# Optimization experiments

Hardware: AMD Instinct MI355X
Metric: run time of the kernel (lower is better)

Reference implementation:

```python
import jax, jax.numpy as jnp
import numpy as np

NEG_INF = -9e15  # matches torch's -9000000000000000.0 mask value
ALPHA = 0.2      # LeakyReLU negative slope


def setup_inputs() -> dict:
    key = jax.random.key(0)
    k1, k2, k3, k4 = jax.random.split(key, 4)
    B, N, Fin, Fout, H = 32, 512, 256, 64, 8
    x = jax.random.normal(k1, (B, N, Fin), dtype=jnp.float32)
    adj = (jax.random.uniform(k2, (B, N, N)) < 0.5).astype(jnp.float32)
    # W: Linear(in_features, out_features*n_heads, bias=False) weight, stored as (Fin, Fout*H)
    W = jax.random.normal(k3, (Fin, Fout * H), dtype=jnp.float32) / np.sqrt(Fin).astype(np.float32)
    # a: attention vector per head over concat(src,dst) features -> (H, 2*Fout)
    a = jax.random.normal(k4, (H, 2 * Fout), dtype=jnp.float32) * 0.1
    return {"x": x, "adj": adj, "W": W, "a": a}


def reference(x, adj, W, a):
    # x: (B,N,Fin), adj: (B,N,N), W: (Fin, H*F), a: (H, 2F)
    B, N, _ = x.shape
    H, twoF = a.shape
    F = twoF // 2
    h = (x @ W).reshape(B, N, H, F)  # (B,N,H,F)
    # Decompose concat-score: e_ij = lrelu(h_i . a_src + h_j . a_dst) -- same math
    # as (cat(h_i,h_j) * a).sum(-1) without materializing (B,N,N,H,2F).
    s_src = jnp.einsum('bnhf,hf->bnh', h, a[:, :F])  # (B,N,H)
    s_dst = jnp.einsum('bnhf,hf->bnh', h, a[:, F:])  # (B,N,H)
    e = s_src[:, :, None, :] + s_dst[:, None, :, :]  # (B,N,N,H)
    e = jax.nn.leaky_relu(e, negative_slope=ALPHA)
    e = jnp.where(adj[..., None] > 0, e, NEG_INF)
    attn = jax.nn.softmax(e, axis=2)  # softmax over neighbors j (dim=2)
    # dropout omitted (eval mode / p effectively 0 for the reference baseline)
    h_prime = jnp.einsum('bijh,bjhf->bihf', attn, h)  # (B,N,H,F)
    return h_prime.reshape(B, N, H * F)  # concat=True
```

## Files before the change

kernel.cpp:

```cpp
#include <hip/hip_runtime.h>
#include <hip/hip_bf16.h>
#include <stdint.h>


#define ALPHA  0.2f
#define ESCALE 1.4426950408889634f

typedef __bf16 bf16x8 __attribute__((ext_vector_type(8)));
typedef __bf16 bf16x4 __attribute__((ext_vector_type(4)));
typedef float  f32x4  __attribute__((ext_vector_type(4)));

#if __has_builtin(__builtin_amdgcn_exp2f)
#define EXP2(x) __builtin_amdgcn_exp2f(x)
#else
#define EXP2(x) exp2f(x)
#endif

#define HT_STRIDE 520
#define WT_STRIDE 264

__device__ inline bf16x8 ld8(const float* p) {
    float4 a0 = *(const float4*)p;
    float4 a1 = *(const float4*)(p + 4);
    bf16x8 r;
    r[0]=(__bf16)a0.x; r[1]=(__bf16)a0.y; r[2]=(__bf16)a0.z; r[3]=(__bf16)a0.w;
    r[4]=(__bf16)a1.x; r[5]=(__bf16)a1.y; r[6]=(__bf16)a1.z; r[7]=(__bf16)a1.w;
    return r;
}

__global__ __launch_bounds__(512) void k0_mask(const float* __restrict__ adj,
                                               unsigned* __restrict__ mask) {
    const int T2 = blockIdx.x * 512 + threadIdx.x;
    const int w    = T2 & 3;
    const int quad = (T2 >> 2) & 3;
    const int row  = (T2 >> 4) & 511;
    const int b    = T2 >> 13;
    const float* p = adj + ((long)b * 512 + row) * 512 + quad * 8;
    unsigned word = 0;
    #pragma unroll
    for (int k = 0; k < 4; ++k) {
        const float* qp = p + (w * 4 + k) * 32;
        float4 a0 = *(const float4*)qp;
        float4 a1 = *(const float4*)(qp + 4);
        unsigned byte =  (a0.x > 0.f ? 1u : 0u)
                      | ((a0.y > 0.f ? 1u : 0u) << 1)
                      | ((a0.z > 0.f ? 1u : 0u) << 2)
                      | ((a0.w > 0.f ? 1u : 0u) << 3)
                      | ((a1.x > 0.f ? 1u : 0u) << 4)
                      | ((a1.y > 0.f ? 1u : 0u) << 5)
                      | ((a1.z > 0.f ? 1u : 0u) << 6)
                      | ((a1.w > 0.f ? 1u : 0u) << 7);
        word |= byte << (8 * k);
    }
    mask[T2] = word;
}

struct SmemK1 {
    __bf16 WT[64][WT_STRIDE];
    float  asrc[64], adst[64];
};

__global__ __launch_bounds__(512, 4) void k1_gemm(const float* __restrict__ x,
                                                  const float* __restrict__ W,
                                                  const float* __restrict__ a,
                                                  __bf16* __restrict__ hT,
                                                  float* __restrict__ ssrc,
                                                  float* __restrict__ sdst) {
    __shared__ SmemK1 sm;
    const int b = blockIdx.x, h = blockIdx.y;
    const int tid  = threadIdx.x;
    const int wave = tid >> 6, lane = tid & 63;
    const int quad = lane >> 4, col = lane & 15;

    if (tid < 128) {
        float v = a[h * 128 + tid] * ESCALE;
        if (tid < 64) sm.asrc[tid] = v; else sm.adst[tid - 64] = v;
    }
    {
        int c = tid & 63, k0 = tid >> 6;
        #pragma unroll 4
        for (int t = 0; t < 32; ++t)
            sm.WT[c][k0 + t * 8] = (__bf16)W[(long)(k0 + t * 8) * 512 + h * 64 + c];
    }
    __syncthreads();

    f32x4 acc[4][4] = {};
    {
        const float* xb = x + (long)b * 512 * 256;
        for (int ks = 0; ks < 8; ++ks) {
            int k0 = ks * 32 + quad * 8;
            bf16x8 av[4], bv[4];
            #pragma unroll
            for (int it = 0; it < 4; ++it)
                av[it] = ld8(xb + (long)(wave * 64 + it * 16 + col) * 256 + k0);
            #pragma unroll
            for (int nt = 0; nt < 4; ++nt)
                bv[nt] = *(const bf16x8*)(&sm.WT[nt * 16 + col][k0]);
            #pragma unroll
            for (int it = 0; it < 4; ++it)
                #pragma unroll
                for (int nt = 0; nt < 4; ++nt)
                    acc[it][nt] = __builtin_amdgcn_mfma_f32_16x16x32_bf16(av[it], bv[nt], acc[it][nt], 0, 0, 0);
        }
    }

    const long bh = (long)b * 8 + h;
    {
        #pragma unroll
        for (int it = 0; it < 4; ++it)
            #pragma unroll
            for (int nt = 0; nt < 4; ++nt) {
                int f = nt * 16 + col;
                int j = wave * 64 + it * 16 + quad * 4;
                bf16x4 pk = { (__bf16)acc[it][nt][0], (__bf16)acc[it][nt][1],
                              (__bf16)acc[it][nt][2], (__bf16)acc[it][nt][3] };
                *(bf16x4*)(hT + (bh * 64 + f) * HT_STRIDE + j) = pk;
            }
    }

    {
        float asr[4], adr[4];
        #pragma unroll
        for (int nt = 0; nt < 4; ++nt) {
            asr[nt] = sm.asrc[nt * 16 + col];
            adr[nt] = sm.adst[nt * 16 + col];
        }
        #pragma unroll
        for (int it = 0; it < 4; ++it)
            #pragma unroll
            for (int r = 0; r < 4; ++r) {
                float ps = 0.f, pd = 0.f;
                #pragma unroll
                for (int nt = 0; nt < 4; ++nt) {
                    ps += acc[it][nt][r] * asr[nt];
                    pd += acc[it][nt][r] * adr[nt];
                }
                #pragma unroll
                for (int m = 1; m <= 8; m <<= 1) {
                    ps += __shfl_xor(ps, m, 64);
                    pd += __shfl_xor(pd, m, 64);
                }
                if (col == 0) {
                    int j = wave * 64 + it * 16 + quad * 4 + r;
                    ssrc[bh * 512 + j] = ps;
                    sdst[bh * 512 + j] = pd;
                }
            }
    }
}

struct SmemK2 {
    __bf16 hT[64][HT_STRIDE];
    float  sds[512];
};

__global__ __launch_bounds__(512, 4) void k2_attn(const uint4* __restrict__ mask,
                                                  const __bf16* __restrict__ hT,
                                                  const float* __restrict__ ssrc,
                                                  const float* __restrict__ sdst,
                                                  float* __restrict__ out) {
    __shared__ SmemK2 sm;
    const int b = blockIdx.x, h = blockIdx.y, q = blockIdx.z;
    const int tid  = threadIdx.x;
    const int wave = tid >> 6, lane = tid & 63;
    const int quad = lane >> 4, col = lane & 15;
    const long bh = (long)b * 8 + h;
    const int rowbase = q * 256 + wave * 32;

    {
        const uint4* src = (const uint4*)(hT + bh * 64 * HT_STRIDE);
        uint4* dst = (uint4*)&sm.hT[0][0];
        #pragma unroll
        for (int t = 0; t < 8; ++t)
            dst[t * 512 + tid] = src[t * 512 + tid];
        if (tid < 64) dst[4096 + tid] = src[4096 + tid];
    }
    sm.sds[tid] = sdst[bh * 512 + tid];

    float si[2]; uint4 mk[2];
    #pragma unroll
    for (int it = 0; it < 2; ++it) {
        int i = rowbase + it * 16 + col;
        si[it] = ssrc[bh * 512 + i];
        mk[it] = mask[((long)b * 512 + i) * 4 + quad];
    }
    __syncthreads();

    bf16x8 ones;
    #pragma unroll
    for (int u = 0; u < 8; ++u) ones[u] = (__bf16)1.0f;

    f32x4 acc[2][4] = {};
    f32x4 accs[2]   = {};

    #pragma unroll
    for (int ks = 0; ks < 16; ++ks) {
        const int j0 = ks * 32 + quad * 8;
        f32x4 s0 = *(const f32x4*)&sm.sds[j0];
        f32x4 s1 = *(const f32x4*)&sm.sds[j0 + 4];
        float sd[8] = {s0[0],s0[1],s0[2],s0[3],s1[0],s1[1],s1[2],s1[3]};
        unsigned mb[2];
        #pragma unroll
        for (int it = 0; it < 2; ++it) {
            unsigned wrd = (ks < 4) ? mk[it].x : (ks < 8) ? mk[it].y
                         : (ks < 12) ? mk[it].z : mk[it].w;
            mb[it] = (wrd >> ((ks & 3) * 8)) & 0xFFu;
        }
        bf16x8 P[2];
        #pragma unroll
        for (int it = 0; it < 2; ++it)
            #pragma unroll
            for (int u = 0; u < 8; ++u) {
                float e = si[it] + sd[u];
                float l = fmaxf(e, ALPHA * e);
                float xv = EXP2(l);
                P[it][u] = (__bf16)(((mb[it] >> u) & 1u) ? xv : 0.0f);
            }
        bf16x8 bv[4];
        #pragma unroll
        for (int nt = 0; nt < 4; ++nt)
            bv[nt] = *(const bf16x8*)(&sm.hT[nt * 16 + col][j0]);
        #pragma unroll
        for (int it = 0; it < 2; ++it) {
            #pragma unroll
            for (int nt = 0; nt < 4; ++nt)
                acc[it][nt] = __builtin_amdgcn_mfma_f32_16x16x32_bf16(P[it], bv[nt], acc[it][nt], 0, 0, 0);
            accs[it] = __builtin_amdgcn_mfma_f32_16x16x32_bf16(P[it], ones, accs[it], 0, 0, 0);
        }
    }
    #pragma unroll
    for (int it = 0; it < 2; ++it)
        #pragma unroll
        for (int r = 0; r < 4; ++r) {
            float s = accs[it][r];
            float inv = (s > 0.f) ? 1.0f / s : 0.f;
            int i = rowbase + it * 16 + quad * 4 + r;
            float* orow = out + ((long)b * 512 + i) * 512 + h * 64;
            #pragma unroll
            for (int nt = 0; nt < 4; ++nt)
                orow[nt * 16 + col] = acc[it][nt][r] * inv;
        }
}

struct SmemF {
    __bf16 hT[64][HT_STRIDE];
    __bf16 WT[64][WT_STRIDE];
    float  ssrc[512], sdst[512];
    float  asrc[64], adst[64];
};

__global__ __launch_bounds__(1024, 4) void k_gat_fused(const float* __restrict__ x,
                                                       const float* __restrict__ adj,
                                                       const float* __restrict__ W,
                                                       const float* __restrict__ a,
                                                       float* __restrict__ out) {
    __shared__ SmemF sm;
    const int b = blockIdx.x, h = blockIdx.y;
    const int tid  = threadIdx.x;
    const int wave = tid >> 6, lane = tid & 63;
    const int quad = lane >> 4, col = lane & 15;

    if (tid < 128) {
        float v = a[h * 128 + tid] * ESCALE;
        if (tid < 64) sm.asrc[tid] = v; else sm.adst[tid - 64] = v;
    }
    {
        int c = tid & 63, k0 = tid >> 6;
        #pragma unroll 4
        for (int t = 0; t < 16; ++t)
            sm.WT[c][k0 + t * 16] = (__bf16)W[(long)(k0 + t * 16) * 512 + h * 64 + c];
    }
    __syncthreads();
    {
        const float* xb = x + (long)b * 512 * 256;
        f32x4 acc[2][4] = {};
        for (int ks = 0; ks < 8; ++ks) {
            int k0 = ks * 32 + quad * 8;
            bf16x8 av[2], bv[4];
            #pragma unroll
            for (int it = 0; it < 2; ++it)
                av[it] = ld8(xb + (long)(wave * 32 + it * 16 + col) * 256 + k0);
            #pragma unroll
            for (int nt = 0; nt < 4; ++nt)
                bv[nt] = *(const bf16x8*)(&sm.WT[nt * 16 + col][k0]);
            #pragma unroll
            for (int it = 0; it < 2; ++it)
                #pragma unroll
                for (int nt = 0; nt < 4; ++nt)
                    acc[it][nt] = __builtin_amdgcn_mfma_f32_16x16x32_bf16(av[it], bv[nt], acc[it][nt], 0, 0, 0);
        }
        #pragma unroll
        for (int it = 0; it < 2; ++it)
            #pragma unroll
            for (int nt = 0; nt < 4; ++nt) {
                int f = nt * 16 + col;
                int j = wave * 32 + it * 16 + quad * 4;
                bf16x4 pk = { (__bf16)acc[it][nt][0], (__bf16)acc[it][nt][1],
                              (__bf16)acc[it][nt][2], (__bf16)acc[it][nt][3] };
                *(bf16x4*)(&sm.hT[f][j]) = pk;
            }
    }
    __syncthreads();
    {
        int j = tid & 511;
        float s = 0.f;
        if (tid < 512) {
            #pragma unroll 8
            for (int f = 0; f < 64; ++f) s += (float)sm.hT[f][j] * sm.asrc[f];
            sm.ssrc[j] = s;
        } else {
            #pragma unroll 8
            for (int f = 0; f < 64; ++f) s += (float)sm.hT[f][j] * sm.adst[f];
            sm.sdst[j] = s;
        }
    }
    __syncthreads();
    {
        float si[2];
        const float* arow[2];
        #pragma unroll
        for (int it = 0; it < 2; ++it) {
            int i = wave * 32 + it * 16 + col;
            si[it]   = sm.ssrc[i];
            arow[it] = adj + ((long)b * 512 + i) * 512;
        }
        bf16x8 ones;
        #pragma unroll
        for (int u = 0; u < 8; ++u) ones[u] = (__bf16)1.0f;
        f32x4 acc[2][4] = {};
        f32x4 accs[2]   = {};
        float4 pa0[2], pa1[2];
        #pragma unroll
        for (int it = 0; it < 2; ++it) {
            pa0[it] = *(const float4*)(arow[it] + quad * 8);
            pa1[it] = *(const float4*)(arow[it] + quad * 8 + 4);
        }
        for (int ks = 0; ks < 16; ++ks) {
            int j0 = ks * 32 + quad * 8;
            f32x4 s0 = *(const f32x4*)&sm.sdst[j0];
            f32x4 s1 = *(const f32x4*)&sm.sdst[j0 + 4];
            float sd[8] = {s0[0],s0[1],s0[2],s0[3],s1[0],s1[1],s1[2],s1[3]};
            float am[2][8];
            #pragma unroll
            for (int it = 0; it < 2; ++it) {
                am[it][0]=pa0[it].x; am[it][1]=pa0[it].y;
                am[it][2]=pa0[it].z; am[it][3]=pa0[it].w;
                am[it][4]=pa1[it].x; am[it][5]=pa1[it].y;
                am[it][6]=pa1[it].z; am[it][7]=pa1[it].w;
            }
            if (ks < 15) {
                #pragma unroll
                for (int it = 0; it < 2; ++it) {
                    pa0[it] = *(const float4*)(arow[it] + j0 + 32);
                    pa1[it] = *(const float4*)(arow[it] + j0 + 36);
                }
            }
            bf16x8 P[2];
            #pragma unroll
            for (int it = 0; it < 2; ++it)
                #pragma unroll
                for (int u = 0; u < 8; ++u) {
                    float e = si[it] + sd[u];
                    float l = fmaxf(e, ALPHA * e);
                    float p = am[it][u] * EXP2(l);
                    P[it][u] = (__bf16)p;
                }
            bf16x8 bv[4];
            #pragma unroll
            for (int nt = 0; nt < 4; ++nt)
                bv[nt] = *(const bf16x8*)(&sm.hT[nt * 16 + col][j0]);
            #pragma unroll
            for (int it = 0; it < 2; ++it) {
                #pragma unroll
                for (int nt = 0; nt < 4; ++nt)
                    acc[it][nt] = __builtin_amdgcn_mfma_f32_16x16x32_bf16(P[it], bv[nt], acc[it][nt], 0, 0, 0);
                accs[it] = __builtin_amdgcn_mfma_f32_16x16x32_bf16(P[it], ones, accs[it], 0, 0, 0);
            }
        }
        #pragma unroll
        for (int it = 0; it < 2; ++it)
            #pragma unroll
            for (int r = 0; r < 4; ++r) {
                float s = accs[it][r];
                float inv = (s > 0.f) ? 1.0f / s : 0.f;
                int i = wave * 32 + it * 16 + quad * 4 + r;
                float* orow = out + ((long)b * 512 + i) * 512 + h * 64;
                #pragma unroll
                for (int nt = 0; nt < 4; ++nt)
                    orow[nt * 16 + col] = acc[it][nt][r] * inv;
            }
    }
}

extern "C" void kernel_launch(void* const* d_in, const int* in_sizes, int n_in,
                              void* d_out, int out_size, void* d_ws, size_t ws_size,
                              hipStream_t stream) {
    const float* x   = (const float*)d_in[0];
    const float* adj = (const float*)d_in[1];
    const float* W   = (const float*)d_in[2];
    const float* a   = (const float*)d_in[3];
    float* out = (float*)d_out;

    const size_t HT_BYTES   = 256ull * 64 * HT_STRIDE * 2;
    const size_t SC_BYTES   = 32ull * 8 * 512 * 4;
    const size_t MASK_BYTES = 32ull * 512 * 64;
    const size_t NEED = HT_BYTES + 2 * SC_BYTES + MASK_BYTES;

    if (d_ws && ws_size >= NEED) {
        __bf16* hT   = (__bf16*)d_ws;
        float* ssrc  = (float*)((char*)d_ws + HT_BYTES);
        float* sdst  = ssrc + 32 * 8 * 512;
        unsigned* mk = (unsigned*)((char*)d_ws + HT_BYTES + 2 * SC_BYTES);
        k0_mask<<<512, 512, 0, stream>>>(adj, mk);
        k1_gemm<<<dim3(32, 8), 512, 0, stream>>>(x, W, a, hT, ssrc, sdst);
        k2_attn<<<dim3(32, 8, 2), 512, 0, stream>>>((const uint4*)mk, hT, ssrc, sdst, out);
    } else {
        k_gat_fused<<<dim3(32, 8), 1024, 0, stream>>>(x, adj, W, a, out);
    }
}
```

Before: 150.6 us.

## Split GEMM kernel rows across four blocks and prefetch x before W staging

The projection kernel now launches four times as many blocks, each handling 128 rows instead of 512, so each wave computes one 16-row tile instead of four. The wave's whole slice of x is loaded into registers at kernel start, before W is staged into shared memory, so global load latency overlaps the shared-memory fill. In exchange, each of the four blocks per (batch, head) reloads and transposes W into shared memory, and the prefetch holds 64 floats of x per thread in registers.

```diff
diff --git a/kernel.cpp b/kernel.cpp
--- a/kernel.cpp
+++ b/kernel.cpp
@@ -67,10 +67,19 @@
                                                   float* __restrict__ ssrc,
                                                   float* __restrict__ sdst) {
     __shared__ SmemK1 sm;
-    const int b = blockIdx.x, h = blockIdx.y;
+    const int b = blockIdx.x, h = blockIdx.y, q4 = blockIdx.z;
     const int tid  = threadIdx.x;
     const int wave = tid >> 6, lane = tid & 63;
     const int quad = lane >> 4, col = lane & 15;
+    const int rbase = q4 * 128 + wave * 16;
+
+    const float* xr = x + ((long)b * 512 + rbase + col) * 256;
+    float4 raw[8][2];
+    #pragma unroll
+    for (int ks = 0; ks < 8; ++ks) {
+        raw[ks][0] = *(const float4*)(xr + ks * 32 + quad * 8);
+        raw[ks][1] = *(const float4*)(xr + ks * 32 + quad * 8 + 4);
+    }
 
     if (tid < 128) {
         float v = a[h * 128 + tid] * ESCALE;
@@ -84,38 +93,34 @@
     }
     __syncthreads();
 
-    f32x4 acc[4][4] = {};
-    {
-        const float* xb = x + (long)b * 512 * 256;
-        for (int ks = 0; ks < 8; ++ks) {
-            int k0 = ks * 32 + quad * 8;
-            bf16x8 av[4], bv[4];
-            #pragma unroll
-            for (int it = 0; it < 4; ++it)
-                av[it] = ld8(xb + (long)(wave * 64 + it * 16 + col) * 256 + k0);
-            #pragma unroll
-            for (int nt = 0; nt < 4; ++nt)
-                bv[nt] = *(const bf16x8*)(&sm.WT[nt * 16 + col][k0]);
-            #pragma unroll
-            for (int it = 0; it < 4; ++it)
-                #pragma unroll
-                for (int nt = 0; nt < 4; ++nt)
-                    acc[it][nt] = __builtin_amdgcn_mfma_f32_16x16x32_bf16(av[it], bv[nt], acc[it][nt], 0, 0, 0);
-        }
+    f32x4 acc[4] = {};
+    #pragma unroll
+    for (int ks = 0; ks < 8; ++ks) {
+        const int k0 = ks * 32 + quad * 8;
+        bf16x8 bv[4];
+        #pragma unroll
+        for (int nt = 0; nt < 4; ++nt)
+            bv[nt] = *(const bf16x8*)(&sm.WT[nt * 16 + col][k0]);
+        bf16x8 av;
+        av[0]=(__bf16)raw[ks][0].x; av[1]=(__bf16)raw[ks][0].y;
+        av[2]=(__bf16)raw[ks][0].z; av[3]=(__bf16)raw[ks][0].w;
+        av[4]=(__bf16)raw[ks][1].x; av[5]=(__bf16)raw[ks][1].y;
+        av[6]=(__bf16)raw[ks][1].z; av[7]=(__bf16)raw[ks][1].w;
+        #pragma unroll
+        for (int nt = 0; nt < 4; ++nt)
+            acc[nt] = __builtin_amdgcn_mfma_f32_16x16x32_bf16(av, bv[nt], acc[nt], 0, 0, 0);
     }
 
     const long bh = (long)b * 8 + h;
     {
         #pragma unroll
-        for (int it = 0; it < 4; ++it)
-            #pragma unroll
-            for (int nt = 0; nt < 4; ++nt) {
-                int f = nt * 16 + col;
-                int j = wave * 64 + it * 16 + quad * 4;
-                bf16x4 pk = { (__bf16)acc[it][nt][0], (__bf16)acc[it][nt][1],
-                              (__bf16)acc[it][nt][2], (__bf16)acc[it][nt][3] };
-                *(bf16x4*)(hT + (bh * 64 + f) * HT_STRIDE + j) = pk;
-            }
+        for (int nt = 0; nt < 4; ++nt) {
+            int f = nt * 16 + col;
+            int j = rbase + quad * 4;
+            bf16x4 pk = { (__bf16)acc[nt][0], (__bf16)acc[nt][1],
+                          (__bf16)acc[nt][2], (__bf16)acc[nt][3] };
+            *(bf16x4*)(hT + (bh * 64 + f) * HT_STRIDE + j) = pk;
+        }
     }
 
     {
@@ -126,26 +131,24 @@
             adr[nt] = sm.adst[nt * 16 + col];
         }
         #pragma unroll
-        for (int it = 0; it < 4; ++it)
-            #pragma unroll
-            for (int r = 0; r < 4; ++r) {
-                float ps = 0.f, pd = 0.f;
-                #pragma unroll
-                for (int nt = 0; nt < 4; ++nt) {
-                    ps += acc[it][nt][r] * asr[nt];
-                    pd += acc[it][nt][r] * adr[nt];
-                }
-                #pragma unroll
-                for (int m = 1; m <= 8; m <<= 1) {
-                    ps += __shfl_xor(ps, m, 64);
-                    pd += __shfl_xor(pd, m, 64);
-                }
-                if (col == 0) {
-                    int j = wave * 64 + it * 16 + quad * 4 + r;
-                    ssrc[bh * 512 + j] = ps;
-                    sdst[bh * 512 + j] = pd;
-                }
-            }
+        for (int r = 0; r < 4; ++r) {
+            float ps = 0.f, pd = 0.f;
+            #pragma unroll
+            for (int nt = 0; nt < 4; ++nt) {
+                ps += acc[nt][r] * asr[nt];
+                pd += acc[nt][r] * adr[nt];
+            }
+            #pragma unroll
+            for (int m = 1; m <= 8; m <<= 1) {
+                ps += __shfl_xor(ps, m, 64);
+                pd += __shfl_xor(pd, m, 64);
+            }
+            if (col == 0) {
+                int j = rbase + quad * 4 + r;
+                ssrc[bh * 512 + j] = ps;
+                sdst[bh * 512 + j] = pd;
+            }
+        }
     }
 }
 
@@ -412,7 +415,7 @@
         float* sdst  = ssrc + 32 * 8 * 512;
         unsigned* mk = (unsigned*)((char*)d_ws + HT_BYTES + 2 * SC_BYTES);
         k0_mask<<<512, 512, 0, stream>>>(adj, mk);
-        k1_gemm<<<dim3(32, 8), 512, 0, stream>>>(x, W, a, hT, ssrc, sdst);
+        k1_gemm<<<dim3(32, 8, 4), 512, 0, stream>>>(x, W, a, hT, ssrc, sdst);
         k2_attn<<<dim3(32, 8, 2), 512, 0, stream>>>((const uint4*)mk, hT, ssrc, sdst, out);
     } else {
         k_gat_fused<<<dim3(32, 8), 1024, 0, stream>>>(x, adj, W, a, out);
```

After: 159.4 us. 1.06x slower.

## Pre-convert x and W to bf16 in mask kernel and tile GEMM through LDS

Applied to the files above, without the earlier changes.

The mask kernel becomes a combined prep kernel that also converts x to bf16 in a k-chunked layout and writes a transposed bf16 copy of W. The GEMM kernel then stages swizzled bf16 tiles of W and x in shared memory instead of loading fp32 x straight from global memory and converting it per head. It also splits rows across two blocks per (batch, head) so more blocks run. In exchange it adds a bf16 x round trip through the workspace and extra barriers while x chunks are reloaded.

```diff
diff --git a/kernel.cpp b/kernel.cpp
--- a/kernel.cpp
+++ b/kernel.cpp
@@ -28,96 +28,165 @@
     return r;
 }
 
-__global__ __launch_bounds__(512) void k0_mask(const float* __restrict__ adj,
-                                               unsigned* __restrict__ mask) {
-    const int T2 = blockIdx.x * 512 + threadIdx.x;
-    const int w    = T2 & 3;
-    const int quad = (T2 >> 2) & 3;
-    const int row  = (T2 >> 4) & 511;
-    const int b    = T2 >> 13;
-    const float* p = adj + ((long)b * 512 + row) * 512 + quad * 8;
-    unsigned word = 0;
-    #pragma unroll
-    for (int k = 0; k < 4; ++k) {
-        const float* qp = p + (w * 4 + k) * 32;
-        float4 a0 = *(const float4*)qp;
-        float4 a1 = *(const float4*)(qp + 4);
-        unsigned byte =  (a0.x > 0.f ? 1u : 0u)
-                      | ((a0.y > 0.f ? 1u : 0u) << 1)
-                      | ((a0.z > 0.f ? 1u : 0u) << 2)
-                      | ((a0.w > 0.f ? 1u : 0u) << 3)
-                      | ((a1.x > 0.f ? 1u : 0u) << 4)
-                      | ((a1.y > 0.f ? 1u : 0u) << 5)
-                      | ((a1.z > 0.f ? 1u : 0u) << 6)
-                      | ((a1.w > 0.f ? 1u : 0u) << 7);
-        word |= byte << (8 * k);
-    }
-    mask[T2] = word;
+__global__ __launch_bounds__(512) void k0_all(const float* __restrict__ x,
+                                              const float* __restrict__ W,
+                                              const float* __restrict__ adj,
+                                              __bf16* __restrict__ xbf,
+                                              __bf16* __restrict__ Wbf,
+                                              unsigned* __restrict__ mask) {
+    __shared__ float tile[64][65];
+    const int blk = blockIdx.x, tid = threadIdx.x;
+    if (blk < 1024) {
+        long c = (long)blk * 512 + tid;
+        int s  = (int)(c & 7);
+        int r  = (int)((c >> 3) & 511);
+        int kc = (int)((c >> 12) & 3);
+        int b  = (int)(c >> 14);
+        const float* src = x + (((long)b * 512 + r) * 256 + kc * 64 + s * 8);
+        float4 a0 = *(const float4*)src;
+        float4 a1 = *(const float4*)(src + 4);
+        bf16x8 o;
+        o[0]=(__bf16)a0.x; o[1]=(__bf16)a0.y; o[2]=(__bf16)a0.z; o[3]=(__bf16)a0.w;
+        o[4]=(__bf16)a1.x; o[5]=(__bf16)a1.y; o[6]=(__bf16)a1.z; o[7]=(__bf16)a1.w;
+        *(bf16x8*)(xbf + c * 8) = o;
+    } else if (blk < 1056) {
+        int bi = blk - 1024;
+        int kt = bi & 3, ft = bi >> 2;
+        int ff = tid & 63;
+        #pragma unroll
+        for (int i = 0; i < 8; ++i) {
+            int kk = (tid >> 6) + i * 8;
+            tile[kk][ff] = W[(long)(kt * 64 + kk) * 512 + ft * 64 + ff];
+        }
+        __syncthreads();
+        int kk2 = tid & 63;
+        #pragma unroll
+        for (int i = 0; i < 8; ++i) {
+            int ff2 = (tid >> 6) + i * 8;
+            Wbf[(long)(ft * 64 + ff2) * 256 + kt * 64 + kk2] = (__bf16)tile[kk2][ff2];
+        }
+    } else {
+        const int T2 = (blk - 1056) * 512 + tid;
+        const int w    = T2 & 3;
+        const int quad = (T2 >> 2) & 3;
+        const int row  = (T2 >> 4) & 511;
+        const int b    = T2 >> 13;
+        const float* p = adj + ((long)b * 512 + row) * 512 + quad * 8;
+        unsigned word = 0;
+        #pragma unroll
+        for (int k = 0; k < 4; ++k) {
+            const float* qp = p + (w * 4 + k) * 32;
+            float4 a0 = *(const float4*)qp;
+            float4 a1 = *(const float4*)(qp + 4);
+            unsigned byte =  (a0.x > 0.f ? 1u : 0u)
+                          | ((a0.y > 0.f ? 1u : 0u) << 1)
+                          | ((a0.z > 0.f ? 1u : 0u) << 2)
+                          | ((a0.w > 0.f ? 1u : 0u) << 3)
+                          | ((a1.x > 0.f ? 1u : 0u) << 4)
+                          | ((a1.y > 0.f ? 1u : 0u) << 5)
+                          | ((a1.z > 0.f ? 1u : 0u) << 6)
+                          | ((a1.w > 0.f ? 1u : 0u) << 7);
+            word |= byte << (8 * k);
+        }
+        mask[T2] = word;
+    }
 }
 
 struct SmemK1 {
-    __bf16 WT[64][WT_STRIDE];
+    __bf16 Wt[64 * 256];
+    __bf16 Xt[256 * 64];
     float  asrc[64], adst[64];
 };
 
-__global__ __launch_bounds__(512, 4) void k1_gemm(const float* __restrict__ x,
-                                                  const float* __restrict__ W,
+__global__ __launch_bounds__(512, 4) void k1_gemm(const __bf16* __restrict__ xbf,
+                                                  const __bf16* __restrict__ Wbf,
                                                   const float* __restrict__ a,
                                                   __bf16* __restrict__ hT,
                                                   float* __restrict__ ssrc,
                                                   float* __restrict__ sdst) {
     __shared__ SmemK1 sm;
-    const int b = blockIdx.x, h = blockIdx.y;
+    const int b = blockIdx.x, h = blockIdx.y, zz = blockIdx.z;
     const int tid  = threadIdx.x;
     const int wave = tid >> 6, lane = tid & 63;
     const int quad = lane >> 4, col = lane & 15;
+    const int row0 = zz * 256;
 
     if (tid < 128) {
         float v = a[h * 128 + tid] * ESCALE;
         if (tid < 64) sm.asrc[tid] = v; else sm.adst[tid - 64] = v;
     }
     {
-        int c = tid & 63, k0 = tid >> 6;
-        #pragma unroll 4
-        for (int t = 0; t < 32; ++t)
-            sm.WT[c][k0 + t * 8] = (__bf16)W[(long)(k0 + t * 8) * 512 + h * 64 + c];
+        const uint4* src = (const uint4*)(Wbf + (long)h * 64 * 256);
+        #pragma unroll
+        for (int i = 0; i < 4; ++i) {
+            int c = tid + i * 512;
+            int f = c >> 5, s = c & 31;
+            int sw = (s & 24) | ((s & 7) ^ (f & 7));
+            *(uint4*)((char*)sm.Wt + f * 512 + sw * 16) = src[c];
+        }
+    }
+    {
+        const uint4* src = (const uint4*)(xbf + (((long)b * 4 + 0) * 512 + row0) * 64);
+        #pragma unroll
+        for (int i = 0; i < 4; ++i) {
+            int c = tid + i * 512;
+            int r = c >> 3, s = c & 7;
+            *(uint4*)((char*)sm.Xt + r * 128 + ((s ^ (r & 7)) * 16)) = src[c];
+        }
     }
     __syncthreads();
 
-    f32x4 acc[4][4] = {};
-    {
-        const float* xb = x + (long)b * 512 * 256;
-        for (int ks = 0; ks < 8; ++ks) {
-            int k0 = ks * 32 + quad * 8;
-            bf16x8 av[4], bv[4];
-            #pragma unroll
-            for (int it = 0; it < 4; ++it)
-                av[it] = ld8(xb + (long)(wave * 64 + it * 16 + col) * 256 + k0);
-            #pragma unroll
-            for (int nt = 0; nt < 4; ++nt)
-                bv[nt] = *(const bf16x8*)(&sm.WT[nt * 16 + col][k0]);
-            #pragma unroll
-            for (int it = 0; it < 4; ++it)
+    f32x4 acc[2][4] = {};
+    #pragma unroll
+    for (int kc = 0; kc < 4; ++kc) {
+        #pragma unroll
+        for (int sk = 0; sk < 2; ++sk) {
+            bf16x8 av[2], bv[4];
+            #pragma unroll
+            for (int it = 0; it < 2; ++it) {
+                int r = wave * 32 + it * 16 + col;
+                int g = (sk * 4 + quad) ^ (r & 7);
+                av[it] = *(const bf16x8*)((const char*)sm.Xt + r * 128 + g * 16);
+            }
+            #pragma unroll
+            for (int nt = 0; nt < 4; ++nt) {
+                int n = nt * 16 + col;
+                int G = kc * 8 + sk * 4 + quad;
+                int Gs = (G & 24) | ((G & 7) ^ (n & 7));
+                bv[nt] = *(const bf16x8*)((const char*)sm.Wt + n * 512 + Gs * 16);
+            }
+            #pragma unroll
+            for (int it = 0; it < 2; ++it)
                 #pragma unroll
                 for (int nt = 0; nt < 4; ++nt)
                     acc[it][nt] = __builtin_amdgcn_mfma_f32_16x16x32_bf16(av[it], bv[nt], acc[it][nt], 0, 0, 0);
         }
+        if (kc < 3) {
+            __syncthreads();
+            const uint4* src = (const uint4*)(xbf + (((long)b * 4 + kc + 1) * 512 + row0) * 64);
+            #pragma unroll
+            for (int i = 0; i < 4; ++i) {
+                int c = tid + i * 512;
+                int r = c >> 3, s = c & 7;
+                *(uint4*)((char*)sm.Xt + r * 128 + ((s ^ (r & 7)) * 16)) = src[c];
+            }
+            __syncthreads();
+        }
     }
 
     const long bh = (long)b * 8 + h;
     {
         #pragma unroll
-        for (int it = 0; it < 4; ++it)
+        for (int it = 0; it < 2; ++it)
             #pragma unroll
             for (int nt = 0; nt < 4; ++nt) {
                 int f = nt * 16 + col;
-                int j = wave * 64 + it * 16 + quad * 4;
+                int j = row0 + wave * 32 + it * 16 + quad * 4;
                 bf16x4 pk = { (__bf16)acc[it][nt][0], (__bf16)acc[it][nt][1],
                               (__bf16)acc[it][nt][2], (__bf16)acc[it][nt][3] };
                 *(bf16x4*)(hT + (bh * 64 + f) * HT_STRIDE + j) = pk;
             }
     }
-
     {
         float asr[4], adr[4];
         #pragma unroll
@@ -126,7 +195,7 @@
             adr[nt] = sm.adst[nt * 16 + col];
         }
         #pragma unroll
-        for (int it = 0; it < 4; ++it)
+        for (int it = 0; it < 2; ++it)
             #pragma unroll
             for (int r = 0; r < 4; ++r) {
                 float ps = 0.f, pd = 0.f;
@@ -141,7 +210,7 @@
                     pd += __shfl_xor(pd, m, 64);
                 }
                 if (col == 0) {
-                    int j = wave * 64 + it * 16 + quad * 4 + r;
+                    int j = row0 + wave * 32 + it * 16 + quad * 4 + r;
                     ssrc[bh * 512 + j] = ps;
                     sdst[bh * 512 + j] = pd;
                 }
@@ -404,15 +473,21 @@
     const size_t HT_BYTES   = 256ull * 64 * HT_STRIDE * 2;
     const size_t SC_BYTES   = 32ull * 8 * 512 * 4;
     const size_t MASK_BYTES = 32ull * 512 * 64;
-    const size_t NEED = HT_BYTES + 2 * SC_BYTES + MASK_BYTES;
+    const size_t XBF_BYTES  = 32ull * 512 * 256 * 2;
+    const size_t WBF_BYTES  = 512ull * 256 * 2;
+    const size_t NEED = HT_BYTES + 2 * SC_BYTES + MASK_BYTES
+                      + XBF_BYTES + WBF_BYTES;
 
     if (d_ws && ws_size >= NEED) {
-        __bf16* hT   = (__bf16*)d_ws;
-        float* ssrc  = (float*)((char*)d_ws + HT_BYTES);
-        float* sdst  = ssrc + 32 * 8 * 512;
-        unsigned* mk = (unsigned*)((char*)d_ws + HT_BYTES + 2 * SC_BYTES);
-        k0_mask<<<512, 512, 0, stream>>>(adj, mk);
-        k1_gemm<<<dim3(32, 8), 512, 0, stream>>>(x, W, a, hT, ssrc, sdst);
+        char* p = (char*)d_ws;
+        __bf16* hT   = (__bf16*)p;                 p += HT_BYTES;
+        float* ssrc  = (float*)p;                  p += SC_BYTES;
+        float* sdst  = (float*)p;                  p += SC_BYTES;
+        unsigned* mk = (unsigned*)p;               p += MASK_BYTES;
+        __bf16* xbf  = (__bf16*)p;                 p += XBF_BYTES;
+        __bf16* Wbf  = (__bf16*)p;
+        k0_all<<<1568, 512, 0, stream>>>(x, W, adj, xbf, Wbf, mk);
+        k1_gemm<<<dim3(32, 8, 2), 512, 0, stream>>>(xbf, Wbf, a, hT, ssrc, sdst);
         k2_attn<<<dim3(32, 8, 2), 512, 0, stream>>>((const uint4*)mk, hT, ssrc, sdst, out);
     } else {
         k_gat_fused<<<dim3(32, 8), 1024, 0, stream>>>(x, adj, W, a, out);
```

Result: no change. 148.1 us (-1.6%).
